# Optimization experiments

Hardware: AMD Instinct MI355X
Metric: run time of the kernel (lower is better)

## Reference

```python
import jax, jax.numpy as jnp
import numpy as np

B, T, D, H = 4, 2048, 1024, 16
HD = D // H

def setup_inputs() -> dict:
    key = jax.random.key(0)
    ks = jax.random.split(key, 7)
    s = 1.0 / np.sqrt(D)
    return {
        "x": jax.random.normal(ks[0], (B, T, D), dtype=jnp.float32),
        "w_qkv": jax.random.uniform(ks[1], (D, 3 * D), jnp.float32, -s, s),
        "b_qkv": jax.random.uniform(ks[2], (3 * D,), jnp.float32, -s, s),
        "w_proj": jax.random.uniform(ks[3], (D, D), jnp.float32, -s, s),
        "b_proj": jax.random.uniform(ks[4], (D,), jnp.float32, -s, s),
        "ln_gamma": jnp.ones((D,), jnp.float32),
        "ln_beta": jnp.zeros((D,), jnp.float32),
    }

def reference(x, w_qkv, b_qkv, w_proj, b_proj, ln_gamma, ln_beta):
    eps = 1e-5
    scale = HD ** -0.5
    residual = x
    # Pre-norm LayerNorm over last dim
    mu = jnp.mean(x, axis=-1, keepdims=True)
    var = jnp.mean(jnp.square(x - mu), axis=-1, keepdims=True)
    xn = (x - mu) * jax.lax.rsqrt(var + eps) * ln_gamma + ln_beta
    # QKV projection: (B,T,3D) -> (3,B,H,T,HD)
    qkv = xn @ w_qkv + b_qkv
    qkv = qkv.reshape(B, T, 3, H, HD).transpose(2, 0, 3, 1, 4)
    q, k, v = qkv[0], qkv[1], qkv[2]
    # Scaled dot-product attention (full T x T scores, as in source)
    attn = jnp.einsum('bhqd,bhkd->bhqk', q, k) * scale
    attn = jax.nn.softmax(attn, axis=-1)
    out = jnp.einsum('bhqk,bhkd->bhqd', attn, v)
    out = out.transpose(0, 2, 1, 3).reshape(B, T, D)
    out = out @ w_proj + b_proj
    return residual + out
```

## Files before the change

### kernel.cpp

```cpp
#include <hip/hip_runtime.h>
#include <cstdint>
#include <cstddef>

#define B_ 4
#define T_ 2048
#define D_ 1024
#define H_ 16

typedef __attribute__((ext_vector_type(8))) short short8;
typedef __attribute__((ext_vector_type(4))) float f32x4;
typedef __attribute__((ext_vector_type(8))) unsigned short u16x8;

__device__ __forceinline__ unsigned short f2b16(float f) {
  union { float f; unsigned int u; } un; un.f = f;
  unsigned int r = un.u + 0x7fffu + ((un.u >> 16) & 1u);
  return (unsigned short)(r >> 16);
}
__device__ __forceinline__ void async_cp16(const void* g, void* l) {
  __builtin_amdgcn_global_load_lds((const __attribute__((address_space(1))) void*)g,
                                   (__attribute__((address_space(3))) void*)l,
                                   16, 0, 0);
}
__device__ __forceinline__ f32x4 mfma16(short8 a, short8 b, f32x4 c) {
  return __builtin_amdgcn_mfma_f32_16x16x32_bf16(a, b, c, 0, 0, 0);
}

__global__ __launch_bounds__(256) void ln_kernel(const float* __restrict__ x,
                                                 const float* __restrict__ gamma,
                                                 const float* __restrict__ beta,
                                                 unsigned short* __restrict__ xn) {
  const int row = blockIdx.x;
  const int t = threadIdx.x;
  const float4 v = ((const float4*)(x + (size_t)row * D_))[t];
  float s  = v.x + v.y + v.z + v.w;
  float s2 = v.x*v.x + v.y*v.y + v.z*v.z + v.w*v.w;
  #pragma unroll
  for (int off = 32; off > 0; off >>= 1) {
    s  += __shfl_down(s, off);
    s2 += __shfl_down(s2, off);
  }
  __shared__ float sh[8];
  const int wv = t >> 6, lane = t & 63;
  if (lane == 0) { sh[wv] = s; sh[4 + wv] = s2; }
  __syncthreads();
  if (t == 0) {
    float ts  = sh[0] + sh[1] + sh[2] + sh[3];
    float ts2 = sh[4] + sh[5] + sh[6] + sh[7];
    float mu  = ts * (1.0f / D_);
    float var = ts2 * (1.0f / D_) - mu * mu;
    sh[0] = mu;
    sh[1] = rsqrtf(var + 1e-5f);
  }
  __syncthreads();
  const float mu = sh[0], rs = sh[1];
  const float4 g  = ((const float4*)gamma)[t];
  const float4 bb = ((const float4*)beta)[t];
  ushort4 o;
  o.x = f2b16((v.x - mu) * rs * g.x + bb.x);
  o.y = f2b16((v.y - mu) * rs * g.y + bb.y);
  o.z = f2b16((v.z - mu) * rs * g.z + bb.z);
  o.w = f2b16((v.w - mu) * rs * g.w + bb.w);
  ((ushort4*)(xn + (size_t)row * D_))[t] = o;
}

__global__ __launch_bounds__(256) void transpose_cast(const float* __restrict__ w,
                                                      unsigned short* __restrict__ wT,
                                                      int K, int N) {
  __shared__ float tile[32][33];
  const int n0 = blockIdx.x * 32;
  const int k0 = blockIdx.y * 32;
  const int tx = threadIdx.x, ty = threadIdx.y;
  #pragma unroll
  for (int i = 0; i < 32; i += 8)
    tile[ty + i][tx] = w[(size_t)(k0 + ty + i) * N + n0 + tx];
  __syncthreads();
  #pragma unroll
  for (int i = 0; i < 32; i += 8)
    wT[(size_t)(n0 + ty + i) * K + k0 + tx] = f2b16(tile[tx][ty + i]);
}

__global__ __launch_bounds__(256) void transpose_v(const unsigned short* __restrict__ vB,
                                                   unsigned short* __restrict__ vtB) {
  __shared__ unsigned short tile[64 * 66];
  const int tid = threadIdx.x;
  const int bh = blockIdx.x;
  const int t0 = blockIdx.y * 64;
  const int lr = tid >> 2, lc = (tid & 3) * 16;
  const unsigned short* src = vB + ((size_t)bh * T_ + t0) * 64;
  *(u16x8*)&tile[lr * 66 + lc]     = *(const u16x8*)(src + (size_t)lr * 64 + lc);
  *(u16x8*)&tile[lr * 66 + lc + 8] = *(const u16x8*)(src + (size_t)lr * 64 + lc + 8);
  __syncthreads();
  const int dv = tid >> 2, cb = (tid & 3) * 16;
  unsigned short outv[16];
  #pragma unroll
  for (int j = 0; j < 16; ++j) {
    const int c = cb + j;
    const int t = (c & 32) | ((c & 4) << 2) | ((c & 16) >> 1) | ((c & 8) >> 1) | (c & 3);
    outv[j] = tile[t * 66 + dv];
  }
  unsigned short* dst = vtB + ((size_t)bh * 64 + dv) * T_ + t0 + cb;
  *(u16x8*)dst       = *(const u16x8*)&outv[0];
  *(u16x8*)(dst + 8) = *(const u16x8*)&outv[8];
}

template <int MODE, int NN>
__global__ __launch_bounds__(512, 2) void gemm8p(const unsigned short* __restrict__ A,
                                                 const unsigned short* __restrict__ Bt,
                                                 const float* __restrict__ bias,
                                                 const float* __restrict__ resid,
                                                 unsigned short* __restrict__ qB,
                                                 unsigned short* __restrict__ kB,
                                                 unsigned short* __restrict__ vB,
                                                 float* __restrict__ outF) {
  constexpr int K = 1024;
  constexpr int NT = 16;
  __shared__ __align__(16) unsigned short As[16384];
  __shared__ __align__(16) unsigned short Bs[32768];

  const int tid  = threadIdx.x;
  const int lane = tid & 63;
  const int wv   = tid >> 6;
  const int l15  = lane & 15, quad = lane >> 4;
  const int wr   = wv >> 1;
  const int wc   = wv & 1;

  constexpr int CPX = (64 * (NN / 256)) / 8;
  const int w = (blockIdx.x & 7) * CPX + (blockIdx.x >> 3);
  const int tileM = (w & 63) * 128;
  const int tileN = (w >> 6) * 256;

  const int sr  = tid >> 3;
  const int scs = ((tid & 7) ^ (sr & 7)) * 8;
  const unsigned short* gA = A  + (size_t)(tileM + sr) * K + scs;
  const unsigned short* gB = Bt + (size_t)(tileN + sr) * K + scs;

  auto stA = [&](int h, int ko, int wb) {
    async_cp16(gA + (size_t)(h * 64) * K + ko, &As[wb * 8192 + h * 4096 + tid * 8]);
  };
  auto stB = [&](int h, int ko, int wb) {
    const unsigned short* g = gB + (size_t)(h * 128) * K + ko;
    unsigned short* l = &Bs[wb * 16384 + h * 8192 + tid * 8];
    async_cp16(g, l);
    async_cp16(g + (size_t)64 * K, l + 4096);
  };

  const int rA  = wr * 16 + l15;
  const int rB  = wc * 64 + l15;
  const int ck0 = ((0 + quad) ^ (l15 & 7)) * 8;
  const int ck1 = ((4 + quad) ^ (l15 & 7)) * 8;

  f32x4 acc[2][2][4] = {};

  stA(0, 0, 0); stB(0, 0, 0); stB(1, 0, 0); stA(1, 0, 0);
  asm volatile("s_waitcnt vmcnt(3)" ::: "memory");
  asm volatile("s_barrier" ::: "memory");

  #pragma unroll 2
  for (int kt = 0; kt < NT; ++kt) {
    const int buf = kt & 1;
    const unsigned short* Ab = &As[buf * 8192];
    const unsigned short* Bb = &Bs[buf * 16384];
    const int wb = buf ^ 1;
    const bool st = (kt + 1) < NT;
    const int ko = (kt + 1) * 64;

    short8 a[2], b0[4][2], b1[4][2];

    a[0] = *(const short8*)&Ab[rA * 64 + ck0];
    a[1] = *(const short8*)&Ab[rA * 64 + ck1];
    #pragma unroll
    for (int fn = 0; fn < 4; ++fn) {
      b0[fn][0] = *(const short8*)&Bb[(rB + fn * 16) * 64 + ck0];
      b0[fn][1] = *(const short8*)&Bb[(rB + fn * 16) * 64 + ck1];
    }
    if (st) stA(0, ko, wb);
    asm volatile("s_waitcnt lgkmcnt(0)" ::: "memory");
    __builtin_amdgcn_sched_barrier(0);
    __builtin_amdgcn_s_setprio(1);
    #pragma unroll
    for (int fn = 0; fn < 4; ++fn) {
      acc[0][0][fn] = mfma16(a[0], b0[fn][0], acc[0][0][fn]);
      acc[0][0][fn] = mfma16(a[1], b0[fn][1], acc[0][0][fn]);
    }
    __builtin_amdgcn_s_setprio(0);
    if (st) asm volatile("s_waitcnt vmcnt(2)" ::: "memory");
    else    asm volatile("s_waitcnt vmcnt(1)" ::: "memory");
    asm volatile("s_barrier" ::: "memory");

    #pragma unroll
    for (int fn = 0; fn < 4; ++fn) {
      b1[fn][0] = *(const short8*)&Bb[8192 + (rB + fn * 16) * 64 + ck0];
      b1[fn][1] = *(const short8*)&Bb[8192 + (rB + fn * 16) * 64 + ck1];
    }
    if (st) stB(0, ko, wb);
    asm volatile("s_waitcnt lgkmcnt(0)" ::: "memory");
    __builtin_amdgcn_sched_barrier(0);
    __builtin_amdgcn_s_setprio(1);
    #pragma unroll
    for (int fn = 0; fn < 4; ++fn) {
      acc[0][1][fn] = mfma16(a[0], b1[fn][0], acc[0][1][fn]);
      acc[0][1][fn] = mfma16(a[1], b1[fn][1], acc[0][1][fn]);
    }
    __builtin_amdgcn_s_setprio(0);
    if (st) asm volatile("s_waitcnt vmcnt(3)" ::: "memory");
    else    asm volatile("s_waitcnt vmcnt(0)" ::: "memory");
    asm volatile("s_barrier" ::: "memory");

    a[0] = *(const short8*)&Ab[4096 + rA * 64 + ck0];
    a[1] = *(const short8*)&Ab[4096 + rA * 64 + ck1];
    if (st) stB(1, ko, wb);
    asm volatile("s_waitcnt lgkmcnt(0)" ::: "memory");
    __builtin_amdgcn_sched_barrier(0);
    __builtin_amdgcn_s_setprio(1);
    #pragma unroll
    for (int fn = 0; fn < 4; ++fn) {
      acc[1][0][fn] = mfma16(a[0], b0[fn][0], acc[1][0][fn]);
      acc[1][0][fn] = mfma16(a[1], b0[fn][1], acc[1][0][fn]);
    }
    __builtin_amdgcn_s_setprio(0);
    asm volatile("s_barrier" ::: "memory");

    if (st) stA(1, ko, wb);
    __builtin_amdgcn_s_setprio(1);
    #pragma unroll
    for (int fn = 0; fn < 4; ++fn) {
      acc[1][1][fn] = mfma16(a[0], b1[fn][0], acc[1][1][fn]);
      acc[1][1][fn] = mfma16(a[1], b1[fn][1], acc[1][1][fn]);
    }
    __builtin_amdgcn_s_setprio(0);
    if (st) asm volatile("s_waitcnt vmcnt(3)" ::: "memory");
    asm volatile("s_barrier" ::: "memory");
  }

  if constexpr (MODE == 0) {
    unsigned short* E = &As[wv * 1152];
    #pragma unroll
    for (int qm = 0; qm < 2; ++qm) {
      #pragma unroll
      for (int qn = 0; qn < 2; ++qn) {
        const int colBase = tileN + qn * 128 + wc * 64;
        const int rowBase = tileM + qm * 64 + wr * 16;
        #pragma unroll
        for (int fn = 0; fn < 4; ++fn) {
          const int col = colBase + fn * 16 + l15;
          const float bv = bias[col];
          const float sc = (col < 1024) ? 0.180336880f : 1.0f;
          #pragma unroll
          for (int r = 0; r < 4; ++r)
            E[(quad * 4 + r) * 72 + fn * 16 + l15] =
                f2b16((acc[qm][qn][fn][r] + bv) * sc);
        }
        const int secq = colBase >> 10;
        const int hh   = (colBase & 1023) >> 6;
        unsigned short* outSec = (secq == 0) ? qB : (secq == 1) ? kB : vB;
        #pragma unroll
        for (int it = 0; it < 2; ++it) {
          const int lrow = it * 8 + (lane >> 3);
          const int row = rowBase + lrow;
          const int b_ = row >> 11, t = row & 2047;
          const u16x8 val = *(const u16x8*)&E[lrow * 72 + (lane & 7) * 8];
          *(u16x8*)(outSec + ((size_t)(b_ * 16 + hh) * T_ + t) * 64 + (lane & 7) * 8) = val;
        }
      }
    }
  } else {
    #pragma unroll
    for (int qm = 0; qm < 2; ++qm) {
      #pragma unroll
      for (int qn = 0; qn < 2; ++qn) {
        #pragma unroll
        for (int fn = 0; fn < 4; ++fn) {
          const int col = tileN + qn * 128 + wc * 64 + fn * 16 + l15;
          const float bv = bias[col];
          #pragma unroll
          for (int r = 0; r < 4; ++r) {
            const int row = tileM + qm * 64 + wr * 16 + quad * 4 + r;
            const size_t idx = (size_t)row * NN + col;
            outF[idx] = acc[qm][qn][fn][r] + bv + resid[idx];
          }
        }
      }
    }
  }
}

__global__ __launch_bounds__(256, 4) void attn_mfma(const unsigned short* __restrict__ qB,
                                                    const unsigned short* __restrict__ kB,
                                                    const unsigned short* __restrict__ vtB,
                                                    unsigned short* __restrict__ aout) {
  __shared__ unsigned short Ks[2][64 * 64];
  __shared__ unsigned short Vs[2][64 * 64];

  const int tid = threadIdx.x;
  const int bid = blockIdx.x;
  const int bh = bid & 63;
  const int qb = bid >> 6;
  const int b = bh >> 4, h = bh & 15;
  const int wv = tid >> 6, lane = tid & 63;
  const int l15 = lane & 15, quad = lane >> 4;

  const unsigned short* qP = qB  + (size_t)bh * T_ * 64;
  const unsigned short* kP = kB  + (size_t)bh * T_ * 64;
  const unsigned short* vP = vtB + (size_t)bh * 64 * T_;
  const int q0 = qb * 128 + wv * 32;

  short8 qf[2][2];
  #pragma unroll
  for (int mi = 0; mi < 2; ++mi)
    #pragma unroll
    for (int ks = 0; ks < 2; ++ks)
      qf[mi][ks] = *(const short8*)(qP + ((size_t)(q0 + mi * 16 + l15)) * 64 + ks * 32 + quad * 8);

  const short8 onesf = {0x3F80, 0x3F80, 0x3F80, 0x3F80, 0x3F80, 0x3F80, 0x3F80, 0x3F80};
  f32x4 accO[2][5] = {};

  const int lrow  = lane >> 3;
  const int lchnk = (lane & 7) ^ (lrow & 7);
  const size_t kOff0 = (size_t)((wv * 2 + 0) * 8 + lrow) * 64 + lchnk * 8;
  const size_t kOff1 = (size_t)((wv * 2 + 1) * 8 + lrow) * 64 + lchnk * 8;
  const size_t vOff0 = (size_t)((wv * 2 + 0) * 8 + lrow) * T_ + lchnk * 8;
  const size_t vOff1 = (size_t)((wv * 2 + 1) * 8 + lrow) * T_ + lchnk * 8;
  const int lOff0 = (wv * 2 + 0) * 512 + lane * 8;
  const int lOff1 = (wv * 2 + 1) * 512 + lane * 8;

  async_cp16(kP + kOff0, &Ks[0][lOff0]);
  async_cp16(kP + kOff1, &Ks[0][lOff1]);
  async_cp16(vP + vOff0, &Vs[0][lOff0]);
  async_cp16(vP + vOff1, &Vs[0][lOff1]);
  __syncthreads();

  for (int kt = 0; kt < 32; ++kt) {
    const int buf = kt & 1;
    if (kt + 1 < 32) {
      const unsigned short* kg = kP + (size_t)(kt + 1) * 64 * 64;
      const unsigned short* vg = vP + (kt + 1) * 64;
      async_cp16(kg + kOff0, &Ks[buf ^ 1][lOff0]);
      async_cp16(kg + kOff1, &Ks[buf ^ 1][lOff1]);
      async_cp16(vg + vOff0, &Vs[buf ^ 1][lOff0]);
      async_cp16(vg + vOff1, &Vs[buf ^ 1][lOff1]);
    }
    const unsigned short* K_ = Ks[buf];
    const unsigned short* V_ = Vs[buf];

    f32x4 accT[4][2] = {};
    #pragma unroll
    for (int ks = 0; ks < 2; ++ks) {
      #pragma unroll
      for (int cc = 0; cc < 4; ++cc) {
        const short8 kb = *(const short8*)&K_[(cc * 16 + l15) * 64 +
                                              (((ks << 2) | quad) ^ (l15 & 7)) * 8];
        accT[cc][0] = mfma16(kb, qf[0][ks], accT[cc][0]);
        accT[cc][1] = mfma16(kb, qf[1][ks], accT[cc][1]);
      }
    }

    short8 pa[2][2];
    #pragma unroll
    for (int mi = 0; mi < 2; ++mi) {
      #pragma unroll
      for (int ks = 0; ks < 2; ++ks) {
        union { unsigned short u[8]; short8 s; } pk;
        #pragma unroll
        for (int r = 0; r < 4; ++r) {
          union { float f; unsigned int u; } e0, e1;
          e0.f = __builtin_amdgcn_exp2f(accT[2 * ks + 0][mi][r]);
          e1.f = __builtin_amdgcn_exp2f(accT[2 * ks + 1][mi][r]);
          pk.u[r]     = (unsigned short)(e0.u >> 16);
          pk.u[4 + r] = (unsigned short)(e1.u >> 16);
        }
        pa[mi][ks] = pk.s;
      }
    }

    #pragma unroll
    for (int ks = 0; ks < 2; ++ks) {
      short8 vb[4];
      #pragma unroll
      for (int nj = 0; nj < 4; ++nj)
        vb[nj] = *(const short8*)&V_[(nj * 16 + l15) * 64 +
                                     (((ks << 2) | quad) ^ (l15 & 7)) * 8];
      #pragma unroll
      for (int mi = 0; mi < 2; ++mi) {
        #pragma unroll
        for (int nj = 0; nj < 4; ++nj)
          accO[mi][nj] = mfma16(pa[mi][ks], vb[nj], accO[mi][nj]);
        accO[mi][4] = mfma16(pa[mi][ks], onesf, accO[mi][4]);
      }
    }

    __syncthreads();
  }

  #pragma unroll
  for (int mi = 0; mi < 2; ++mi) {
    #pragma unroll
    for (int r = 0; r < 4; ++r) {
      const float inv = 1.0f / accO[mi][4][r];
      const int row = q0 + mi * 16 + quad * 4 + r;
      unsigned short* op = aout + (size_t)(b * T_ + row) * D_ + h * 64 + l15;
      #pragma unroll
      for (int nj = 0; nj < 4; ++nj)
        op[nj * 16] = f2b16(accO[mi][nj][r] * inv);
    }
  }
}

extern "C" void kernel_launch(void* const* d_in, const int* in_sizes, int n_in,
                              void* d_out, int out_size, void* d_ws, size_t ws_size,
                              hipStream_t stream) {
  const float* x      = (const float*)d_in[0];
  const float* w_qkv  = (const float*)d_in[1];
  const float* b_qkv  = (const float*)d_in[2];
  const float* w_proj = (const float*)d_in[3];
  const float* b_proj = (const float*)d_in[4];
  const float* ln_g   = (const float*)d_in[5];
  const float* ln_b   = (const float*)d_in[6];
  float* out = (float*)d_out;

  char* ws = (char*)d_ws;
  unsigned short* xn   = (unsigned short*)(ws);
  unsigned short* wTq  = (unsigned short*)(ws + (size_t)(16 << 20));
  unsigned short* wTp  = (unsigned short*)(ws + (size_t)(22 << 20));
  unsigned short* qBuf = (unsigned short*)(ws + (size_t)(24 << 20));
  unsigned short* kBuf = (unsigned short*)(ws + (size_t)(40 << 20));
  unsigned short* vBuf = (unsigned short*)(ws + (size_t)(56 << 20));
  unsigned short* vtB  = (unsigned short*)(ws + (size_t)(72 << 20));
  unsigned short* aout = xn;

  ln_kernel<<<8192, 256, 0, stream>>>(x, ln_g, ln_b, xn);
  transpose_cast<<<dim3(96, 32), dim3(32, 8), 0, stream>>>(w_qkv, wTq, 1024, 3072);
  transpose_cast<<<dim3(32, 32), dim3(32, 8), 0, stream>>>(w_proj, wTp, 1024, 1024);
  gemm8p<0, 3072><<<768, 512, 0, stream>>>(xn, wTq, b_qkv, nullptr,
                                           qBuf, kBuf, vBuf, nullptr);
  transpose_v<<<dim3(64, 32), 256, 0, stream>>>(vBuf, vtB);
  attn_mfma<<<1024, 256, 0, stream>>>(qBuf, kBuf, vtB, aout);
  gemm8p<1, 1024><<<256, 512, 0, stream>>>(aout, wTp, b_proj, x,
                                           nullptr, nullptr, nullptr, out);
}
```

Measured before the change: 270.2 us.

## Fuse prep kernels, enlarge QKV GEMM tile, write transposed V in epilogue

Merges LayerNorm and both weight transpose-casts into one launch. Replaces the 128x256 QKV GEMM with a 256x256-tile kernel whose epilogue writes V directly in transposed layout, which removes the separate V transpose kernel and its round trip through global memory. The larger tile raises data reuse per block but halves the grid to 384 blocks and doubles the LDS footprint, which may lower occupancy.

```diff
diff --git a/kernel.cpp b/kernel.cpp
--- a/kernel.cpp
+++ b/kernel.cpp
@@ -25,82 +25,276 @@
   return __builtin_amdgcn_mfma_f32_16x16x32_bf16(a, b, c, 0, 0, 0);
 }
 
-__global__ __launch_bounds__(256) void ln_kernel(const float* __restrict__ x,
-                                                 const float* __restrict__ gamma,
-                                                 const float* __restrict__ beta,
-                                                 unsigned short* __restrict__ xn) {
-  const int row = blockIdx.x;
+__global__ __launch_bounds__(256) void prep_kernel(const float* __restrict__ x,
+                                                   const float* __restrict__ gamma,
+                                                   const float* __restrict__ beta,
+                                                   unsigned short* __restrict__ xn,
+                                                   const float* __restrict__ wq,
+                                                   unsigned short* __restrict__ wTq,
+                                                   const float* __restrict__ wp,
+                                                   unsigned short* __restrict__ wTp) {
+  __shared__ float sh[8];
+  __shared__ float tile[32][33];
+  const int bid = blockIdx.x;
   const int t = threadIdx.x;
-  const float4 v = ((const float4*)(x + (size_t)row * D_))[t];
-  float s  = v.x + v.y + v.z + v.w;
-  float s2 = v.x*v.x + v.y*v.y + v.z*v.z + v.w*v.w;
-  #pragma unroll
-  for (int off = 32; off > 0; off >>= 1) {
-    s  += __shfl_down(s, off);
-    s2 += __shfl_down(s2, off);
-  }
-  __shared__ float sh[8];
-  const int wv = t >> 6, lane = t & 63;
-  if (lane == 0) { sh[wv] = s; sh[4 + wv] = s2; }
-  __syncthreads();
-  if (t == 0) {
-    float ts  = sh[0] + sh[1] + sh[2] + sh[3];
-    float ts2 = sh[4] + sh[5] + sh[6] + sh[7];
-    float mu  = ts * (1.0f / D_);
-    float var = ts2 * (1.0f / D_) - mu * mu;
-    sh[0] = mu;
-    sh[1] = rsqrtf(var + 1e-5f);
-  }
-  __syncthreads();
-  const float mu = sh[0], rs = sh[1];
-  const float4 g  = ((const float4*)gamma)[t];
-  const float4 bb = ((const float4*)beta)[t];
-  ushort4 o;
-  o.x = f2b16((v.x - mu) * rs * g.x + bb.x);
-  o.y = f2b16((v.y - mu) * rs * g.y + bb.y);
-  o.z = f2b16((v.z - mu) * rs * g.z + bb.z);
-  o.w = f2b16((v.w - mu) * rs * g.w + bb.w);
-  ((ushort4*)(xn + (size_t)row * D_))[t] = o;
-}
-
-__global__ __launch_bounds__(256) void transpose_cast(const float* __restrict__ w,
-                                                      unsigned short* __restrict__ wT,
-                                                      int K, int N) {
-  __shared__ float tile[32][33];
-  const int n0 = blockIdx.x * 32;
-  const int k0 = blockIdx.y * 32;
-  const int tx = threadIdx.x, ty = threadIdx.y;
-  #pragma unroll
-  for (int i = 0; i < 32; i += 8)
-    tile[ty + i][tx] = w[(size_t)(k0 + ty + i) * N + n0 + tx];
-  __syncthreads();
-  #pragma unroll
-  for (int i = 0; i < 32; i += 8)
-    wT[(size_t)(n0 + ty + i) * K + k0 + tx] = f2b16(tile[tx][ty + i]);
-}
-
-__global__ __launch_bounds__(256) void transpose_v(const unsigned short* __restrict__ vB,
-                                                   unsigned short* __restrict__ vtB) {
-  __shared__ unsigned short tile[64 * 66];
-  const int tid = threadIdx.x;
-  const int bh = blockIdx.x;
-  const int t0 = blockIdx.y * 64;
-  const int lr = tid >> 2, lc = (tid & 3) * 16;
-  const unsigned short* src = vB + ((size_t)bh * T_ + t0) * 64;
-  *(u16x8*)&tile[lr * 66 + lc]     = *(const u16x8*)(src + (size_t)lr * 64 + lc);
-  *(u16x8*)&tile[lr * 66 + lc + 8] = *(const u16x8*)(src + (size_t)lr * 64 + lc + 8);
-  __syncthreads();
-  const int dv = tid >> 2, cb = (tid & 3) * 16;
-  unsigned short outv[16];
-  #pragma unroll
-  for (int j = 0; j < 16; ++j) {
-    const int c = cb + j;
-    const int t = (c & 32) | ((c & 4) << 2) | ((c & 16) >> 1) | ((c & 8) >> 1) | (c & 3);
-    outv[j] = tile[t * 66 + dv];
-  }
-  unsigned short* dst = vtB + ((size_t)bh * 64 + dv) * T_ + t0 + cb;
-  *(u16x8*)dst       = *(const u16x8*)&outv[0];
-  *(u16x8*)(dst + 8) = *(const u16x8*)&outv[8];
+
+  if (bid < 8192) {
+    const int row = bid;
+    const float4 v = ((const float4*)(x + (size_t)row * D_))[t];
+    float s  = v.x + v.y + v.z + v.w;
+    float s2 = v.x*v.x + v.y*v.y + v.z*v.z + v.w*v.w;
+    #pragma unroll
+    for (int off = 32; off > 0; off >>= 1) {
+      s  += __shfl_down(s, off);
+      s2 += __shfl_down(s2, off);
+    }
+    const int wv = t >> 6, lane = t & 63;
+    if (lane == 0) { sh[wv] = s; sh[4 + wv] = s2; }
+    __syncthreads();
+    if (t == 0) {
+      float ts  = sh[0] + sh[1] + sh[2] + sh[3];
+      float ts2 = sh[4] + sh[5] + sh[6] + sh[7];
+      float mu  = ts * (1.0f / D_);
+      float var = ts2 * (1.0f / D_) - mu * mu;
+      sh[0] = mu;
+      sh[1] = rsqrtf(var + 1e-5f);
+    }
+    __syncthreads();
+    const float mu = sh[0], rs = sh[1];
+    const float4 g  = ((const float4*)gamma)[t];
+    const float4 bb = ((const float4*)beta)[t];
+    ushort4 o;
+    o.x = f2b16((v.x - mu) * rs * g.x + bb.x);
+    o.y = f2b16((v.y - mu) * rs * g.y + bb.y);
+    o.z = f2b16((v.z - mu) * rs * g.z + bb.z);
+    o.w = f2b16((v.w - mu) * rs * g.w + bb.w);
+    ((ushort4*)(xn + (size_t)row * D_))[t] = o;
+  } else {
+    const float* w; unsigned short* wT; int K, N, bx, by;
+    if (bid < 8192 + 3072) {
+      const int idx = bid - 8192;
+      w = wq; wT = wTq; K = 1024; N = 3072; bx = idx % 96; by = idx / 96;
+    } else {
+      const int idx = bid - 11264;
+      w = wp; wT = wTp; K = 1024; N = 1024; bx = idx % 32; by = idx / 32;
+    }
+    const int n0 = bx * 32, k0 = by * 32;
+    const int tx = t & 31, ty = t >> 5;
+    #pragma unroll
+    for (int i = 0; i < 32; i += 8)
+      tile[ty + i][tx] = w[(size_t)(k0 + ty + i) * N + n0 + tx];
+    __syncthreads();
+    #pragma unroll
+    for (int i = 0; i < 32; i += 8)
+      wT[(size_t)(n0 + ty + i) * K + k0 + tx] = f2b16(tile[tx][ty + i]);
+  }
+}
+
+__global__ __launch_bounds__(512, 2) void gemm256_qkv(const unsigned short* __restrict__ A,
+                                                      const unsigned short* __restrict__ Bt,
+                                                      const float* __restrict__ bias,
+                                                      unsigned short* __restrict__ qB,
+                                                      unsigned short* __restrict__ kB,
+                                                      unsigned short* __restrict__ vtB) {
+  constexpr int K = 1024;
+  constexpr int NT = K / 64;
+  __shared__ __align__(16) unsigned short As[32768];
+  __shared__ __align__(16) unsigned short Bs[32768];
+
+  const int tid  = threadIdx.x;
+  const int lane = tid & 63;
+  const int wv   = tid >> 6;
+  const int l15  = lane & 15, quad = lane >> 4;
+  const int wr   = wv >> 1;
+  const int wc   = wv & 1;
+
+  const int w = (blockIdx.x & 7) * 48 + (blockIdx.x >> 3);
+  const int tileM = (w & 31) * 256;
+  const int tileN = (w >> 5) * 256;
+
+  const int sr  = tid >> 3;
+  const int scs = ((tid & 7) ^ (sr & 7)) * 8;
+  const unsigned short* gA = A  + (size_t)(tileM + sr) * K + scs;
+  const unsigned short* gB = Bt + (size_t)(tileN + sr) * K + scs;
+
+  auto stageA = [&](int h, int ko, int wbuf) {
+    const unsigned short* g = gA + (size_t)(h * 128) * K + ko;
+    unsigned short* l = &As[wbuf * 16384 + h * 8192 + tid * 8];
+    async_cp16(g, l);
+    async_cp16(g + (size_t)64 * K, l + 4096);
+  };
+  auto stageB = [&](int h, int ko, int wbuf) {
+    const unsigned short* g = gB + (size_t)(h * 128) * K + ko;
+    unsigned short* l = &Bs[wbuf * 16384 + h * 8192 + tid * 8];
+    async_cp16(g, l);
+    async_cp16(g + (size_t)64 * K, l + 4096);
+  };
+
+  const int rA  = wr * 32 + l15;
+  const int rB  = wc * 64 + l15;
+  const int ck0 = ((0 + quad) ^ (l15 & 7)) * 8;
+  const int ck1 = ((4 + quad) ^ (l15 & 7)) * 8;
+
+  f32x4 acc[2][2][2][4] = {};
+
+#define MFMA16(QM, QN, AF, BF)                                                          \
+  do {                                                                                  \
+    _Pragma("unroll") for (int fm = 0; fm < 2; ++fm)                                    \
+    _Pragma("unroll") for (int fn = 0; fn < 4; ++fn) {                                  \
+      acc[QM][QN][fm][fn] = mfma16(AF[fm][0], BF[fn][0], acc[QM][QN][fm][fn]);          \
+      acc[QM][QN][fm][fn] = mfma16(AF[fm][1], BF[fn][1], acc[QM][QN][fm][fn]);          \
+    }                                                                                   \
+  } while (0)
+
+  stageA(0, 0, 0);
+  stageB(0, 0, 0);
+  stageB(1, 0, 0);
+  stageA(1, 0, 0);
+  asm volatile("s_waitcnt vmcnt(4)" ::: "memory");
+  asm volatile("s_barrier" ::: "memory");
+
+  #pragma unroll 2
+  for (int kt = 0; kt < NT; ++kt) {
+    const int buf = kt & 1;
+    const unsigned short* Ab = &As[buf * 16384];
+    const unsigned short* Bb = &Bs[buf * 16384];
+    const int wbuf = buf ^ 1;
+    const bool st = (kt + 1) < NT;
+    const int ko = (kt + 1) * 64;
+
+    short8 a[2][2], b0[4][2], b1[4][2];
+
+    #pragma unroll
+    for (int fm = 0; fm < 2; ++fm) {
+      a[fm][0] = *(const short8*)&Ab[(rA + fm * 16) * 64 + ck0];
+      a[fm][1] = *(const short8*)&Ab[(rA + fm * 16) * 64 + ck1];
+    }
+    #pragma unroll
+    for (int fn = 0; fn < 4; ++fn) {
+      b0[fn][0] = *(const short8*)&Bb[(rB + fn * 16) * 64 + ck0];
+      b0[fn][1] = *(const short8*)&Bb[(rB + fn * 16) * 64 + ck1];
+    }
+    if (st) stageA(0, ko, wbuf);
+    asm volatile("s_waitcnt lgkmcnt(0)" ::: "memory");
+    __builtin_amdgcn_sched_barrier(0);
+    __builtin_amdgcn_s_setprio(1);
+    MFMA16(0, 0, a, b0);
+    __builtin_amdgcn_s_setprio(0);
+    if (st) asm volatile("s_waitcnt vmcnt(4)" ::: "memory");
+    else    asm volatile("s_waitcnt vmcnt(2)" ::: "memory");
+    asm volatile("s_barrier" ::: "memory");
+
+    #pragma unroll
+    for (int fn = 0; fn < 4; ++fn) {
+      b1[fn][0] = *(const short8*)&Bb[8192 + (rB + fn * 16) * 64 + ck0];
+      b1[fn][1] = *(const short8*)&Bb[8192 + (rB + fn * 16) * 64 + ck1];
+    }
+    if (st) stageB(0, ko, wbuf);
+    asm volatile("s_waitcnt lgkmcnt(0)" ::: "memory");
+    __builtin_amdgcn_sched_barrier(0);
+    __builtin_amdgcn_s_setprio(1);
+    MFMA16(0, 1, a, b1);
+    __builtin_amdgcn_s_setprio(0);
+    if (st) asm volatile("s_waitcnt vmcnt(4)" ::: "memory");
+    else    asm volatile("s_waitcnt vmcnt(0)" ::: "memory");
+    asm volatile("s_barrier" ::: "memory");
+
+    #pragma unroll
+    for (int fm = 0; fm < 2; ++fm) {
+      a[fm][0] = *(const short8*)&Ab[8192 + (rA + fm * 16) * 64 + ck0];
+      a[fm][1] = *(const short8*)&Ab[8192 + (rA + fm * 16) * 64 + ck1];
+    }
+    if (st) stageB(1, ko, wbuf);
+    asm volatile("s_waitcnt lgkmcnt(0)" ::: "memory");
+    __builtin_amdgcn_sched_barrier(0);
+    __builtin_amdgcn_s_setprio(1);
+    MFMA16(1, 0, a, b0);
+    __builtin_amdgcn_s_setprio(0);
+    asm volatile("s_barrier" ::: "memory");
+
+    if (st) stageA(1, ko, wbuf);
+    __builtin_amdgcn_s_setprio(1);
+    MFMA16(1, 1, a, b1);
+    __builtin_amdgcn_s_setprio(0);
+    if (st) asm volatile("s_waitcnt vmcnt(4)" ::: "memory");
+    asm volatile("s_barrier" ::: "memory");
+  }
+#undef MFMA16
+
+  if (tileN < 2048) {
+    unsigned short* E = &As[wv * 2304];
+    #pragma unroll
+    for (int qm = 0; qm < 2; ++qm) {
+      #pragma unroll
+      for (int qn = 0; qn < 2; ++qn) {
+        const int colBase = tileN + qn * 128 + wc * 64;
+        const int rowBase = tileM + qm * 128 + wr * 32;
+        #pragma unroll
+        for (int fn = 0; fn < 4; ++fn) {
+          const int col = colBase + fn * 16 + l15;
+          const float bv = bias[col];
+          const float sc = (col < 1024) ? 0.180336880f : 1.0f;
+          #pragma unroll
+          for (int fm = 0; fm < 2; ++fm)
+            #pragma unroll
+            for (int r = 0; r < 4; ++r)
+              E[(fm * 16 + quad * 4 + r) * 72 + fn * 16 + l15] =
+                  f2b16((acc[qm][qn][fm][fn][r] + bv) * sc);
+        }
+        const int secq = colBase >> 10;
+        const int hh   = (colBase & 1023) >> 6;
+        unsigned short* outSec = (secq == 0) ? qB : kB;
+        #pragma unroll
+        for (int it = 0; it < 4; ++it) {
+          const int lrow = it * 8 + (lane >> 3);
+          const int row = rowBase + lrow;
+          const int b_ = row >> 11, tt = row & 2047;
+          const u16x8 val = *(const u16x8*)&E[lrow * 72 + (lane & 7) * 8];
+          *(u16x8*)(outSec + ((size_t)(b_ * 16 + hh) * T_ + tt) * 64 + (lane & 7) * 8) = val;
+        }
+      }
+    }
+  } else {
+    const int b_    = tileM >> 11;
+    const int tbase = tileM & 2047;
+    const int h0    = (tileN - 2048) >> 6;
+    unsigned short* TL = (wr < 2) ? As : Bs;
+    const int cpr = 32 * (wr & 1) + 8 * quad;
+    #pragma unroll
+    for (int qm = 0; qm < 2; ++qm) {
+      #pragma unroll
+      for (int qn = 0; qn < 2; ++qn) {
+        const int head = qn * 2 + wc;
+        const int colBase = tileN + qn * 128 + wc * 64;
+        #pragma unroll
+        for (int fn = 0; fn < 4; ++fn) {
+          const int dv = fn * 16 + l15;
+          const float bv = bias[colBase + fn * 16 + l15];
+          #pragma unroll
+          for (int fm = 0; fm < 2; ++fm)
+            #pragma unroll
+            for (int r = 0; r < 4; ++r)
+              TL[head * 4352 + dv * 68 + cpr + 4 * fm + r] =
+                  f2b16(acc[qm][qn][fm][fn][r] + bv);
+        }
+      }
+      __syncthreads();
+      {
+        const unsigned short* SA = (wv < 4) ? As : Bs;
+        const int head = wv & 3;
+        const int tb   = qm * 2 + (wv >> 2);
+        const size_t base = ((size_t)(b_ * 16 + h0 + head) * 64) * T_ + tbase + tb * 64;
+        const int c4 = (lane & 15) * 4;
+        #pragma unroll
+        for (int i = 0; i < 16; ++i) {
+          const int dv = i * 4 + (lane >> 4);
+          const ushort4 val = *(const ushort4*)&SA[head * 4352 + dv * 68 + c4];
+          *(ushort4*)(vtB + base + (size_t)dv * T_ + c4) = val;
+        }
+      }
+      __syncthreads();
+    }
+  }
 }
 
 template <int MODE, int NN>
@@ -108,9 +302,6 @@
                                                  const unsigned short* __restrict__ Bt,
                                                  const float* __restrict__ bias,
                                                  const float* __restrict__ resid,
-                                                 unsigned short* __restrict__ qB,
-                                                 unsigned short* __restrict__ kB,
-                                                 unsigned short* __restrict__ vB,
                                                  float* __restrict__ outF) {
   constexpr int K = 1024;
   constexpr int NT = 16;
@@ -232,52 +423,19 @@
     asm volatile("s_barrier" ::: "memory");
   }
 
-  if constexpr (MODE == 0) {
-    unsigned short* E = &As[wv * 1152];
-    #pragma unroll
-    for (int qm = 0; qm < 2; ++qm) {
-      #pragma unroll
-      for (int qn = 0; qn < 2; ++qn) {
-        const int colBase = tileN + qn * 128 + wc * 64;
-        const int rowBase = tileM + qm * 64 + wr * 16;
-        #pragma unroll
-        for (int fn = 0; fn < 4; ++fn) {
-          const int col = colBase + fn * 16 + l15;
-          const float bv = bias[col];
-          const float sc = (col < 1024) ? 0.180336880f : 1.0f;
-          #pragma unroll
-          for (int r = 0; r < 4; ++r)
-            E[(quad * 4 + r) * 72 + fn * 16 + l15] =
-                f2b16((acc[qm][qn][fn][r] + bv) * sc);
-        }
-        const int secq = colBase >> 10;
-        const int hh   = (colBase & 1023) >> 6;
-        unsigned short* outSec = (secq == 0) ? qB : (secq == 1) ? kB : vB;
-        #pragma unroll
-        for (int it = 0; it < 2; ++it) {
-          const int lrow = it * 8 + (lane >> 3);
-          const int row = rowBase + lrow;
-          const int b_ = row >> 11, t = row & 2047;
-          const u16x8 val = *(const u16x8*)&E[lrow * 72 + (lane & 7) * 8];
-          *(u16x8*)(outSec + ((size_t)(b_ * 16 + hh) * T_ + t) * 64 + (lane & 7) * 8) = val;
-        }
-      }
-    }
-  } else {
-    #pragma unroll
-    for (int qm = 0; qm < 2; ++qm) {
-      #pragma unroll
-      for (int qn = 0; qn < 2; ++qn) {
-        #pragma unroll
-        for (int fn = 0; fn < 4; ++fn) {
-          const int col = tileN + qn * 128 + wc * 64 + fn * 16 + l15;
-          const float bv = bias[col];
-          #pragma unroll
-          for (int r = 0; r < 4; ++r) {
-            const int row = tileM + qm * 64 + wr * 16 + quad * 4 + r;
-            const size_t idx = (size_t)row * NN + col;
-            outF[idx] = acc[qm][qn][fn][r] + bv + resid[idx];
-          }
+  #pragma unroll
+  for (int qm = 0; qm < 2; ++qm) {
+    #pragma unroll
+    for (int qn = 0; qn < 2; ++qn) {
+      #pragma unroll
+      for (int fn = 0; fn < 4; ++fn) {
+        const int col = tileN + qn * 128 + wc * 64 + fn * 16 + l15;
+        const float bv = bias[col];
+        #pragma unroll
+        for (int r = 0; r < 4; ++r) {
+          const int row = tileM + qm * 64 + wr * 16 + quad * 4 + r;
+          const size_t idx = (size_t)row * NN + col;
+          outF[idx] = acc[qm][qn][fn][r] + bv + resid[idx];
         }
       }
     }
@@ -423,17 +581,11 @@
   unsigned short* wTp  = (unsigned short*)(ws + (size_t)(22 << 20));
   unsigned short* qBuf = (unsigned short*)(ws + (size_t)(24 << 20));
   unsigned short* kBuf = (unsigned short*)(ws + (size_t)(40 << 20));
-  unsigned short* vBuf = (unsigned short*)(ws + (size_t)(56 << 20));
   unsigned short* vtB  = (unsigned short*)(ws + (size_t)(72 << 20));
   unsigned short* aout = xn;
 
-  ln_kernel<<<8192, 256, 0, stream>>>(x, ln_g, ln_b, xn);
-  transpose_cast<<<dim3(96, 32), dim3(32, 8), 0, stream>>>(w_qkv, wTq, 1024, 3072);
-  transpose_cast<<<dim3(32, 32), dim3(32, 8), 0, stream>>>(w_proj, wTp, 1024, 1024);
-  gemm8p<0, 3072><<<768, 512, 0, stream>>>(xn, wTq, b_qkv, nullptr,
-                                           qBuf, kBuf, vBuf, nullptr);
-  transpose_v<<<dim3(64, 32), 256, 0, stream>>>(vBuf, vtB);
+  prep_kernel<<<12288, 256, 0, stream>>>(x, ln_g, ln_b, xn, w_qkv, wTq, w_proj, wTp);
+  gemm256_qkv<<<384, 512, 0, stream>>>(xn, wTq, b_qkv, qBuf, kBuf, vtB);
   attn_mfma<<<1024, 256, 0, stream>>>(qBuf, kBuf, vtB, aout);
-  gemm8p<1, 1024><<<256, 512, 0, stream>>>(aout, wTp, b_proj, x,
-                                           nullptr, nullptr, nullptr, out);
-}
+  gemm8p<1, 1024><<<256, 512, 0, stream>>>(aout, wTp, b_proj, x, out);
+}
```

New measurement: 268.6 us. No clear change (-0.6%).
